# Performance work log

Measured on AMD Instinct MI355X. Metric: run time of the kernel, lower is better.

## Reference

```python
import jax, jax.numpy as jnp
import numpy as np

BLKPT = 1.0     # black-point percentile
WHTPT = 99.0    # white-point percentile
MAX_MULT = 1.5  # cap on brightening multiplier


def setup_inputs() -> dict:
    key = jax.random.key(0)
    # [B, 3, H, W] image in [0, 1]
    image = jax.random.uniform(key, (16, 3, 1024, 1024), dtype=jnp.float32)
    # standard BT.601 RGB->YUV matrix (module buffer RGB2YUV)
    rgb2yuv = jnp.array([[0.299, 0.587, 0.114],
                         [-0.14713, -0.28886, 0.436],
                         [0.615, -0.51499, -0.10001]], dtype=jnp.float32)
    return {"image": image, "rgb2yuv": rgb2yuv}


def reference(image, rgb2yuv):
    # Only the Y (luma) channel of the YUV conversion is consumed, so we
    # contract with the first matrix row instead of materializing full YUV.
    y = jnp.einsum('j,bjhw->bhw', rgb2yuv[0], image)        # [B, H, W]
    yf = y.reshape(y.shape[0], -1)                          # [B, H*W]
    blkpt = jnp.percentile(yf, BLKPT, axis=1)               # [B]
    whtpt = jnp.percentile(yf, WHTPT, axis=1)               # [B]
    mult = jnp.minimum(1.0 / (whtpt - blkpt), MAX_MULT)     # max_mult > 0 branch
    blkpt = blkpt[:, None, None, None]
    mult = mult[:, None, None, None]
    return jnp.clip((image - blkpt) * mult, 0.0, 1.0)
```

## Files before the change

### kernel.cpp

```cpp
#include <hip/hip_runtime.h>

#define NPIX (1024 * 1024)
#define NBATCH 16
#define NBINS 8192
#define SUBPB 64
#define HTHREADS 512
#define PIXPB (NPIX / SUBPB)

typedef float vfloat4 __attribute__((ext_vector_type(4)));

__global__ void zero_kernel(unsigned int* __restrict__ g) {
    int i = blockIdx.x * blockDim.x + threadIdx.x;
    int n = NBATCH * NBINS;
    for (; i < n; i += gridDim.x * blockDim.x) g[i] = 0u;
}

__global__ __launch_bounds__(HTHREADS) void hist_kernel(
        const float* __restrict__ img,
        const float* __restrict__ rgb2yuv,
        unsigned int* __restrict__ ghist) {
    __shared__ unsigned int lh[NBINS];
    for (int i = threadIdx.x; i < NBINS; i += HTHREADS) lh[i] = 0;
    const float c0 = rgb2yuv[0];
    const float c1 = rgb2yuv[1];
    const float c2 = rgb2yuv[2];
    __syncthreads();

    const int b = blockIdx.x / SUBPB;
    const int s = blockIdx.x % SUBPB;
    const size_t base = (size_t)b * 3 * NPIX + (size_t)s * PIXPB;

    const float4* r4 = (const float4*)(img + base);
    const float4* g4 = (const float4*)(img + base + NPIX);
    const float4* b4 = (const float4*)(img + base + 2 * (size_t)NPIX);
    const int t = threadIdx.x;
    const float scale = (float)NBINS;

    float4 Ra = r4[t], Ga = g4[t], Ba = b4[t];
    float4 Rb = r4[t + HTHREADS], Gb = g4[t + HTHREADS], Bb = b4[t + HTHREADS];

#pragma unroll
    for (int k = 0; k < 8; ++k) {
        float4 Rc = {0.f, 0.f, 0.f, 0.f};
        float4 Gc = {0.f, 0.f, 0.f, 0.f};
        float4 Bc = {0.f, 0.f, 0.f, 0.f};
        if (k + 2 < 8) {
            int j = t + (k + 2) * HTHREADS;
            Rc = r4[j];
            Gc = g4[j];
            Bc = b4[j];
        }
        float y0 = c0 * Ra.x + c1 * Ga.x + c2 * Ba.x;
        float y1 = c0 * Ra.y + c1 * Ga.y + c2 * Ba.y;
        float y2 = c0 * Ra.z + c1 * Ga.z + c2 * Ba.z;
        float y3 = c0 * Ra.w + c1 * Ga.w + c2 * Ba.w;
        int i0 = min(NBINS - 1, max(0, (int)(y0 * scale)));
        int i1 = min(NBINS - 1, max(0, (int)(y1 * scale)));
        int i2 = min(NBINS - 1, max(0, (int)(y2 * scale)));
        int i3 = min(NBINS - 1, max(0, (int)(y3 * scale)));
        atomicAdd(&lh[i0], 1u);
        atomicAdd(&lh[i1], 1u);
        atomicAdd(&lh[i2], 1u);
        atomicAdd(&lh[i3], 1u);
        Ra = Rb; Ga = Gb; Ba = Bb;
        Rb = Rc; Gb = Gc; Bb = Bc;
    }
    __syncthreads();

    unsigned int* dst = ghist + (size_t)b * NBINS;
    for (int i = t; i < NBINS; i += HTHREADS) {
        unsigned int v = lh[i];
        if (v) atomicAdd(&dst[i], v);
    }
}

__global__ __launch_bounds__(1024) void scan_kernel(
        const unsigned int* __restrict__ ghist,
        float* __restrict__ stats) {
    __shared__ unsigned int hist[NBINS];
    __shared__ unsigned int segsum[1024];
    __shared__ float vals[4];

    const int b = blockIdx.x;
    const int t = threadIdx.x;

    for (int i = t; i < NBINS; i += 1024)
        hist[i] = ghist[(size_t)b * NBINS + i];
    __syncthreads();

    const int BPT = NBINS / 1024;
    unsigned int ss = 0;
#pragma unroll
    for (int j = 0; j < BPT; ++j) ss += hist[t * BPT + j];
    segsum[t] = ss;
    __syncthreads();

    for (int off = 1; off < 1024; off <<= 1) {
        unsigned int v = segsum[t];
        unsigned int add = (t >= off) ? segsum[t - off] : 0u;
        __syncthreads();
        segsum[t] = v + add;
        __syncthreads();
    }

    const unsigned int cumincl = segsum[t];
    const unsigned int cumbefore = (t > 0) ? segsum[t - 1] : 0u;

    const unsigned int ranks[4] = {10485u, 10486u, 1038089u, 1038090u};
#pragma unroll
    for (int q = 0; q < 4; ++q) {
        unsigned int r = ranks[q];
        if (r >= cumbefore && r < cumincl) {
            unsigned int running = cumbefore;
#pragma unroll
            for (int j = 0; j < BPT; ++j) {
                unsigned int c = hist[t * BPT + j];
                if (r < running + c) {
                    vals[q] = ((float)(t * BPT + j) +
                               ((float)(r - running) + 0.5f) / (float)c) *
                              (1.0f / (float)NBINS);
                    break;
                }
                running += c;
            }
        }
    }
    __syncthreads();

    if (t == 0) {
        float blk = 0.25f * vals[0] + 0.75f * vals[1];
        float wht = 0.75f * vals[2] + 0.25f * vals[3];
        float mult = fminf(1.0f / (wht - blk), 1.5f);
        stats[b * 2 + 0] = blk;
        stats[b * 2 + 1] = mult;
    }
}

__global__ __launch_bounds__(256) void apply_kernel(
        const float* __restrict__ img,
        const float* __restrict__ stats,
        float* __restrict__ out) {
    const int blocksPerBatch = (3 * NPIX / 4) / 1024;
    const int b = blockIdx.x / blocksPerBatch;
    const int c = blockIdx.x % blocksPerBatch;
    const float blk = stats[b * 2 + 0];
    const float mult = stats[b * 2 + 1];

    const vfloat4* in4 =
        (const vfloat4*)(img + (size_t)b * 3 * NPIX) + (size_t)c * 1024;
    vfloat4* out4 = (vfloat4*)(out + (size_t)b * 3 * NPIX) + (size_t)c * 1024;

    const int t = threadIdx.x;
    vfloat4 v0 = in4[t];
    vfloat4 v1 = in4[t + 256];
    vfloat4 v2 = in4[t + 512];
    vfloat4 v3 = in4[t + 768];

#define CLIP1(vv)                                          \
    vv.x = fminf(fmaxf((vv.x - blk) * mult, 0.0f), 1.0f);  \
    vv.y = fminf(fmaxf((vv.y - blk) * mult, 0.0f), 1.0f);  \
    vv.z = fminf(fmaxf((vv.z - blk) * mult, 0.0f), 1.0f);  \
    vv.w = fminf(fmaxf((vv.w - blk) * mult, 0.0f), 1.0f)
    CLIP1(v0);
    CLIP1(v1);
    CLIP1(v2);
    CLIP1(v3);
#undef CLIP1

    out4[t] = v0;
    out4[t + 256] = v1;
    out4[t + 512] = v2;
    out4[t + 768] = v3;
}

extern "C" void kernel_launch(void* const* d_in, const int* in_sizes, int n_in,
                              void* d_out, int out_size, void* d_ws, size_t ws_size,
                              hipStream_t stream) {
    const float* img = (const float*)d_in[0];
    const float* rgb2yuv = (const float*)d_in[1];
    float* out = (float*)d_out;

    float* stats = (float*)d_ws;
    unsigned int* ghist = (unsigned int*)((char*)d_ws + 256);

    zero_kernel<<<128, 256, 0, stream>>>(ghist);
    hist_kernel<<<NBATCH * SUBPB, HTHREADS, 0, stream>>>(img, rgb2yuv, ghist);
    scan_kernel<<<NBATCH, 1024, 0, stream>>>(ghist, stats);

    const int applyBlocks = NBATCH * ((3 * NPIX / 4) / 1024);
    apply_kernel<<<applyBlocks, 256, 0, stream>>>(img, stats, out);
}
```

Measured before the change: 375.1 us.

## Replace shared-memory privatized histogram with direct global atomics

The histogram kernel no longer builds a per-block shared-memory histogram that is merged into global memory. Each pixel now issues an atomic add straight to the global per-batch histogram, launched with many more small blocks of 256 threads. This removes the LDS zeroing, the block barriers and the final merge, but sends about 16M global atomics into only 8192 bins per batch, so heavy contention and L2 atomic throughput are likely to become the bottleneck.

```diff
diff --git a/kernel.cpp b/kernel.cpp
--- a/kernel.cpp
+++ b/kernel.cpp
@@ -3,9 +3,6 @@
 #define NPIX (1024 * 1024)
 #define NBATCH 16
 #define NBINS 8192
-#define SUBPB 64
-#define HTHREADS 512
-#define PIXPB (NPIX / SUBPB)
 
 typedef float vfloat4 __attribute__((ext_vector_type(4)));
 
@@ -15,63 +12,50 @@
     for (; i < n; i += gridDim.x * blockDim.x) g[i] = 0u;
 }
 
-__global__ __launch_bounds__(HTHREADS) void hist_kernel(
+__global__ __launch_bounds__(256) void hist_kernel(
         const float* __restrict__ img,
         const float* __restrict__ rgb2yuv,
         unsigned int* __restrict__ ghist) {
-    __shared__ unsigned int lh[NBINS];
-    for (int i = threadIdx.x; i < NBINS; i += HTHREADS) lh[i] = 0;
+    const int blocksPerBatch = (NPIX / 4) / 1024;
+    const int b = blockIdx.x / blocksPerBatch;
+    const int c = blockIdx.x % blocksPerBatch;
     const float c0 = rgb2yuv[0];
     const float c1 = rgb2yuv[1];
     const float c2 = rgb2yuv[2];
-    __syncthreads();
 
-    const int b = blockIdx.x / SUBPB;
-    const int s = blockIdx.x % SUBPB;
-    const size_t base = (size_t)b * 3 * NPIX + (size_t)s * PIXPB;
+    const size_t base = (size_t)b * 3 * NPIX;
+    const float4* r4 = (const float4*)(img + base) + (size_t)c * 1024;
+    const float4* g4 = (const float4*)(img + base + NPIX) + (size_t)c * 1024;
+    const float4* b4 =
+        (const float4*)(img + base + 2 * (size_t)NPIX) + (size_t)c * 1024;
+    unsigned int* h = ghist + (size_t)b * NBINS;
 
-    const float4* r4 = (const float4*)(img + base);
-    const float4* g4 = (const float4*)(img + base + NPIX);
-    const float4* b4 = (const float4*)(img + base + 2 * (size_t)NPIX);
     const int t = threadIdx.x;
+    float4 R0 = r4[t], R1 = r4[t + 256], R2 = r4[t + 512], R3 = r4[t + 768];
+    float4 G0 = g4[t], G1 = g4[t + 256], G2 = g4[t + 512], G3 = g4[t + 768];
+    float4 B0 = b4[t], B1 = b4[t + 256], B2 = b4[t + 512], B3 = b4[t + 768];
+
     const float scale = (float)NBINS;
-
-    float4 Ra = r4[t], Ga = g4[t], Ba = b4[t];
-    float4 Rb = r4[t + HTHREADS], Gb = g4[t + HTHREADS], Bb = b4[t + HTHREADS];
-
-#pragma unroll
-    for (int k = 0; k < 8; ++k) {
-        float4 Rc = {0.f, 0.f, 0.f, 0.f};
-        float4 Gc = {0.f, 0.f, 0.f, 0.f};
-        float4 Bc = {0.f, 0.f, 0.f, 0.f};
-        if (k + 2 < 8) {
-            int j = t + (k + 2) * HTHREADS;
-            Rc = r4[j];
-            Gc = g4[j];
-            Bc = b4[j];
-        }
-        float y0 = c0 * Ra.x + c1 * Ga.x + c2 * Ba.x;
-        float y1 = c0 * Ra.y + c1 * Ga.y + c2 * Ba.y;
-        float y2 = c0 * Ra.z + c1 * Ga.z + c2 * Ba.z;
-        float y3 = c0 * Ra.w + c1 * Ga.w + c2 * Ba.w;
-        int i0 = min(NBINS - 1, max(0, (int)(y0 * scale)));
-        int i1 = min(NBINS - 1, max(0, (int)(y1 * scale)));
-        int i2 = min(NBINS - 1, max(0, (int)(y2 * scale)));
-        int i3 = min(NBINS - 1, max(0, (int)(y3 * scale)));
-        atomicAdd(&lh[i0], 1u);
-        atomicAdd(&lh[i1], 1u);
-        atomicAdd(&lh[i2], 1u);
-        atomicAdd(&lh[i3], 1u);
-        Ra = Rb; Ga = Gb; Ba = Bb;
-        Rb = Rc; Gb = Gc; Bb = Bc;
+#define HIST4(R, G, B)                                                 \
+    {                                                                  \
+        float y0 = c0 * R.x + c1 * G.x + c2 * B.x;                     \
+        float y1 = c0 * R.y + c1 * G.y + c2 * B.y;                     \
+        float y2 = c0 * R.z + c1 * G.z + c2 * B.z;                     \
+        float y3 = c0 * R.w + c1 * G.w + c2 * B.w;                     \
+        int i0 = min(NBINS - 1, max(0, (int)(y0 * scale)));            \
+        int i1 = min(NBINS - 1, max(0, (int)(y1 * scale)));            \
+        int i2 = min(NBINS - 1, max(0, (int)(y2 * scale)));            \
+        int i3 = min(NBINS - 1, max(0, (int)(y3 * scale)));            \
+        atomicAdd(&h[i0], 1u);                                         \
+        atomicAdd(&h[i1], 1u);                                         \
+        atomicAdd(&h[i2], 1u);                                         \
+        atomicAdd(&h[i3], 1u);                                         \
     }
-    __syncthreads();
-
-    unsigned int* dst = ghist + (size_t)b * NBINS;
-    for (int i = t; i < NBINS; i += HTHREADS) {
-        unsigned int v = lh[i];
-        if (v) atomicAdd(&dst[i], v);
-    }
+    HIST4(R0, G0, B0);
+    HIST4(R1, G1, B1);
+    HIST4(R2, G2, B2);
+    HIST4(R3, G3, B3);
+#undef HIST4
 }
 
 __global__ __launch_bounds__(1024) void scan_kernel(
@@ -184,7 +168,10 @@
     unsigned int* ghist = (unsigned int*)((char*)d_ws + 256);
 
     zero_kernel<<<128, 256, 0, stream>>>(ghist);
-    hist_kernel<<<NBATCH * SUBPB, HTHREADS, 0, stream>>>(img, rgb2yuv, ghist);
+
+    const int histBlocks = NBATCH * ((NPIX / 4) / 1024);
+    hist_kernel<<<histBlocks, 256, 0, stream>>>(img, rgb2yuv, ghist);
+
     scan_kernel<<<NBATCH, 1024, 0, stream>>>(ghist, stats);
 
     const int applyBlocks = NBATCH * ((3 * NPIX / 4) / 1024);
```

After: 1.256 ms. +234.8%, slower.
